# Kernel tuning notes

Measured on AMD Instinct MI355X. Metric: run time of the kernel, lower is better.

## Reference

```python
import jax, jax.numpy as jnp
import numpy as np

GROUPS = 8
EPS = 1e-3  # keras GroupNormalization default epsilon


def group_norm(x, gamma, beta):
    # Keras GroupNormalization(axis=-1): reduce over all non-batch, non-group axes.
    B, L, C = x.shape
    xg = x.reshape(B, L, GROUPS, C // GROUPS)
    mean = jnp.mean(xg, axis=(1, 3), keepdims=True)          # [B,1,G,1]
    var = jnp.var(xg, axis=(1, 3), keepdims=True)
    xn = ((xg - mean) * jax.lax.rsqrt(var + EPS)).reshape(B, L, C)
    return xn * gamma + beta


def setup_inputs() -> dict:
    key = jax.random.key(0)
    ks = jax.random.split(key, 6)
    B, L, C = 8, 2048, 512
    x = jax.random.normal(ks[0], (B, L, C), dtype=jnp.float32)
    s = 0.02
    return {
        "x": x,
        "gamma": jnp.ones((C,), jnp.float32),
        "beta": jnp.zeros((C,), jnp.float32),
        "wq": jax.random.normal(ks[1], (C, C), jnp.float32) * s,
        "bq": jnp.zeros((C,), jnp.float32),
        "wk": jax.random.normal(ks[2], (C, C), jnp.float32) * s,
        "bk": jnp.zeros((C,), jnp.float32),
        "wv": jax.random.normal(ks[3], (C, C), jnp.float32) * s,
        "bv": jnp.zeros((C,), jnp.float32),
        "wp": jax.random.normal(ks[4], (C, C), jnp.float32) * s,
        "bp": jnp.zeros((C,), jnp.float32),
    }


def reference(x, gamma, beta, wq, bq, wk, bk, wv, bv, wp, bp):
    C = x.shape[-1]
    scale = jnp.float32(C) ** -0.5
    h = group_norm(x, gamma, beta)                           # normalized input (also residual!)
    q = h @ wq + bq                                          # [B,L,C]
    k = h @ wk + bk
    v = h @ wv + bv
    attn = jnp.einsum('blc,bLc->blL', q, k) * scale          # [B,L,L]
    attn = jax.nn.softmax(attn, axis=-1)
    o = jnp.einsum('blL,bLc->blc', attn, v)                  # [B,L,C]
    o = o @ wp + bp
    return h + o
```

## Files before the change

### kernel.cpp

```cpp
#include <hip/hip_runtime.h>
#include <hip/hip_bf16.h>
#include <cstdint>

typedef unsigned short ushort_t;
typedef __bf16  bf16x8 __attribute__((ext_vector_type(8)));
typedef float   f32x4  __attribute__((ext_vector_type(4)));

#define L_SEQ 2048
#define C_DIM 512
#define B_SZ  8
#define N_GROUPS 8
#define CG 64

__device__ __forceinline__ float bf2f(ushort_t u) {
    union { uint32_t i; float f; } x; x.i = ((uint32_t)u) << 16; return x.f;
}
__device__ __forceinline__ ushort_t f2bf(float f) {
    union { float f; uint32_t i; } x; x.f = f;
    uint32_t i = x.i;
    uint32_t r = (i + 0x7FFFu + ((i >> 16) & 1u)) >> 16;
    return (ushort_t)r;
}

__device__ __forceinline__ void gl_lds16(const ushort_t* g, ushort_t* l) {
    __builtin_amdgcn_global_load_lds(
        (const __attribute__((address_space(1))) unsigned int*)g,
        (__attribute__((address_space(3))) unsigned int*)l, 16, 0, 0);
}

__global__ __launch_bounds__(256) void conv_stats(const float* __restrict__ wq,
                                                  const float* __restrict__ wk,
                                                  const float* __restrict__ wv,
                                                  const float* __restrict__ wp,
                                                  ushort_t* __restrict__ wqkvT,
                                                  ushort_t* __restrict__ wpT,
                                                  const float* __restrict__ x,
                                                  float* __restrict__ sums) {
    int tid = threadIdx.x;
    if (blockIdx.x < 256) {
        __shared__ ushort_t Ts[64][72];
        int blk = blockIdx.x;
        int mat = blk >> 6, t = blk & 63;
        int k0 = (t >> 3) * 64, n0 = (t & 7) * 64;
        const float* srcs[4] = {wq, wk, wv, wp};
        const float* src = srcs[mat];
        #pragma unroll
        for (int i = 0; i < 2; ++i) {
            int idx = tid * 2 + i;
            int row = idx >> 3, c8 = (idx & 7) * 8;
            const float* p = src + (size_t)(k0 + row) * 512 + n0 + c8;
            float4 a = *(const float4*)p;
            float4 b = *(const float4*)(p + 4);
            Ts[row][c8 + 0] = f2bf(a.x); Ts[row][c8 + 1] = f2bf(a.y);
            Ts[row][c8 + 2] = f2bf(a.z); Ts[row][c8 + 3] = f2bf(a.w);
            Ts[row][c8 + 4] = f2bf(b.x); Ts[row][c8 + 5] = f2bf(b.y);
            Ts[row][c8 + 6] = f2bf(b.z); Ts[row][c8 + 7] = f2bf(b.w);
        }
        __syncthreads();
        int dr = tid >> 2, lc = (tid & 3) * 16;
        union { uint4 v[2]; ushort_t u[16]; } o;
        #pragma unroll
        for (int j = 0; j < 16; ++j) o.u[j] = Ts[lc + j][dr];
        ushort_t* dst = (mat == 3 ? wpT + (size_t)(n0 + dr) * 512
                                  : wqkvT + (size_t)(mat * 512 + n0 + dr) * 512) + k0 + lc;
        *(uint4*)dst = o.v[0];
        *(uint4*)(dst + 8) = o.v[1];
    } else {
        int bid = blockIdx.x - 256;
        int bg = bid >> 3, sp = bid & 7;
        int b = bg >> 3, g = bg & 7;
        const float* base = x + ((size_t)b * L_SEQ + sp * 256) * C_DIM + g * CG;
        float s = 0.f, s2 = 0.f;
        #pragma unroll
        for (int it = 0; it < 8; ++it) {
            int i = it * 2048 + tid * 8;
            int l = i >> 6, c = i & 63;
            const float* p = base + (size_t)l * C_DIM + c;
            float4 a = *(const float4*)p;
            float4 bb = *(const float4*)(p + 4);
            s  += a.x + a.y + a.z + a.w + bb.x + bb.y + bb.z + bb.w;
            s2 += a.x*a.x + a.y*a.y + a.z*a.z + a.w*a.w
                + bb.x*bb.x + bb.y*bb.y + bb.z*bb.z + bb.w*bb.w;
        }
        #pragma unroll
        for (int off = 32; off > 0; off >>= 1) { s += __shfl_down(s, off); s2 += __shfl_down(s2, off); }
        __shared__ float rs[4], rs2[4];
        int wave = tid >> 6;
        if ((tid & 63) == 0) { rs[wave] = s; rs2[wave] = s2; }
        __syncthreads();
        if (tid == 0) {
            sums[bg * 16 + sp * 2 + 0] = rs[0] + rs[1] + rs[2] + rs[3];
            sums[bg * 16 + sp * 2 + 1] = rs2[0] + rs2[1] + rs2[2] + rs2[3];
        }
    }
}

__global__ __launch_bounds__(256) void gn_apply(const float* __restrict__ x,
                                                const float* __restrict__ gamma,
                                                const float* __restrict__ beta,
                                                const float* __restrict__ sums,
                                                ushort_t* __restrict__ h) {
    size_t e = ((size_t)blockIdx.x * 256 + threadIdx.x) * 8;
    int c = (int)(e % C_DIM);
    size_t bl = e / C_DIM;
    int b = (int)(bl / L_SEQ);
    int g = c >> 6;
    int bg = b * 8 + g;
    float s = 0.f, s2 = 0.f;
    #pragma unroll
    for (int sp = 0; sp < 8; ++sp) { s += sums[bg * 16 + sp * 2]; s2 += sums[bg * 16 + sp * 2 + 1]; }
    const float N = (float)(L_SEQ * CG);
    float mean = s / N;
    float var  = s2 / N - mean * mean;
    float rstd = rsqrtf(var + 1e-3f);
    float4 a = *(const float4*)(x + e);
    float4 bb = *(const float4*)(x + e + 4);
    float xf[8] = {a.x, a.y, a.z, a.w, bb.x, bb.y, bb.z, bb.w};
    union { uint4 v; ushort_t u[8]; } o;
    #pragma unroll
    for (int i = 0; i < 8; ++i)
        o.u[i] = f2bf((xf[i] - mean) * rstd * gamma[c + i] + beta[c + i]);
    *(uint4*)(h + e) = o.v;
}

__global__ __launch_bounds__(256) void gemm_qkv(const ushort_t* __restrict__ h,
                                                const ushort_t* __restrict__ wqkvT,
                                                const float* __restrict__ bq,
                                                const float* __restrict__ bk,
                                                const float* __restrict__ bv,
                                                ushort_t* __restrict__ qb,
                                                ushort_t* __restrict__ kb,
                                                ushort_t* __restrict__ vtb) {
    __shared__ ushort_t As[128][64];
    __shared__ ushort_t Bs[128][64];
    int id = blockIdx.x;
    const ushort_t *A, *BT;
    int m0, n0g, vmode;
    if (id < 1024) {
        int swz = (id & 7) * 128 + (id >> 3);
        n0g = (swz & 7) * 128;
        m0  = (swz >> 3) * 128;
        A = h; BT = wqkvT; vmode = 0;
    } else {
        int vid = id - 1024;
        int swz = (vid & 7) * 64 + (vid >> 3);
        n0g = (swz >> 2) * 128;
        m0  = (swz & 3) * 128;
        A = wqkvT + 2 * (size_t)C_DIM * C_DIM; BT = h; vmode = 1;
    }
    int tid = threadIdx.x, lane = tid & 63, w = tid >> 6;
    int l15 = lane & 15, quad = lane >> 4;
    int wm = w >> 1, wn = w & 1;
    int lr8 = lane >> 3;
    int gch = (lane & 7) ^ lr8;
    int h8  = l15 & 7;
    f32x4 acc[4][4] = {};
    for (int k0 = 0; k0 < 512; k0 += 64) {
        #pragma unroll
        for (int j = 0; j < 4; ++j) {
            int rb = w * 32 + j * 8;
            int r  = rb + lr8;
            gl_lds16(A  + (size_t)(m0 + r) * 512 + k0 + gch * 8, &As[rb][0]);
            gl_lds16(BT + (size_t)(n0g + r) * 512 + k0 + gch * 8, &Bs[rb][0]);
        }
        __syncthreads();
        #pragma unroll
        for (int kk = 0; kk < 2; ++kk) {
            int slot = ((quad + 4 * kk) ^ h8) * 8;
            bf16x8 af[4], bf[4];
            #pragma unroll
            for (int t = 0; t < 4; ++t) {
                af[t] = *(const bf16x8*)&As[wm * 64 + t * 16 + l15][slot];
                bf[t] = *(const bf16x8*)&Bs[wn * 64 + t * 16 + l15][slot];
            }
            #pragma unroll
            for (int mt = 0; mt < 4; ++mt)
                #pragma unroll
                for (int nt = 0; nt < 4; ++nt)
                    acc[mt][nt] = __builtin_amdgcn_mfma_f32_16x16x32_bf16(af[mt], bf[nt], acc[mt][nt], 0, 0, 0);
        }
        __syncthreads();
    }
    if (vmode == 0) {
        int seg = n0g >> 9;
        const float* bias = seg ? bk : bq;
        ushort_t* ob = seg ? kb : qb;
        int ns = n0g & 511;
        #pragma unroll
        for (int mt = 0; mt < 4; ++mt)
            #pragma unroll
            for (int nt = 0; nt < 4; ++nt) {
                int n = ns + wn * 64 + nt * 16 + l15;
                float bvn = bias[n];
                #pragma unroll
                for (int r = 0; r < 4; ++r) {
                    int m = m0 + wm * 64 + mt * 16 + quad * 4 + r;
                    ob[(size_t)m * 512 + n] = f2bf(acc[mt][nt][r] + bvn);
                }
            }
    } else {
        #pragma unroll
        for (int mt = 0; mt < 4; ++mt)
            #pragma unroll
            for (int nt = 0; nt < 4; ++nt) {
                int n = n0g + wn * 64 + nt * 16 + l15;
                #pragma unroll
                for (int r = 0; r < 4; ++r) {
                    int m = m0 + wm * 64 + mt * 16 + quad * 4 + r;
                    float v = acc[mt][nt][r] + bv[m];
                    vtb[(size_t)(n >> 11) * 1048576 + (size_t)m * 2048 + (n & 2047)] = f2bf(v);
                }
            }
    }
}

__global__ __launch_bounds__(256) void gemm_proj(const ushort_t* __restrict__ A,
                                                 const ushort_t* __restrict__ BT,
                                                 const float* __restrict__ b0,
                                                 const ushort_t* __restrict__ res,
                                                 float* __restrict__ of) {
    __shared__ ushort_t As[128][64];
    __shared__ ushort_t Bs[128][64];
    int id = blockIdx.x;
    int swz = (id & 7) * 64 + (id >> 3);
    int n0g = (swz & 3) * 128;
    int m0  = (swz >> 2) * 128;
    int tid = threadIdx.x, lane = tid & 63, w = tid >> 6;
    int l15 = lane & 15, quad = lane >> 4;
    int wm = w >> 1, wn = w & 1;
    int lr8 = lane >> 3;
    int gch = (lane & 7) ^ lr8;
    int h8  = l15 & 7;
    f32x4 acc[4][4] = {};
    for (int k0 = 0; k0 < 512; k0 += 64) {
        #pragma unroll
        for (int j = 0; j < 4; ++j) {
            int rb = w * 32 + j * 8;
            int r  = rb + lr8;
            gl_lds16(A  + (size_t)(m0 + r) * 512 + k0 + gch * 8, &As[rb][0]);
            gl_lds16(BT + (size_t)(n0g + r) * 512 + k0 + gch * 8, &Bs[rb][0]);
        }
        __syncthreads();
        #pragma unroll
        for (int kk = 0; kk < 2; ++kk) {
            int slot = ((quad + 4 * kk) ^ h8) * 8;
            bf16x8 af[4], bf[4];
            #pragma unroll
            for (int t = 0; t < 4; ++t) {
                af[t] = *(const bf16x8*)&As[wm * 64 + t * 16 + l15][slot];
                bf[t] = *(const bf16x8*)&Bs[wn * 64 + t * 16 + l15][slot];
            }
            #pragma unroll
            for (int mt = 0; mt < 4; ++mt)
                #pragma unroll
                for (int nt = 0; nt < 4; ++nt)
                    acc[mt][nt] = __builtin_amdgcn_mfma_f32_16x16x32_bf16(af[mt], bf[nt], acc[mt][nt], 0, 0, 0);
        }
        __syncthreads();
    }
    #pragma unroll
    for (int mt = 0; mt < 4; ++mt)
        #pragma unroll
        for (int nt = 0; nt < 4; ++nt) {
            int n = n0g + wn * 64 + nt * 16 + l15;
            float bvn = b0[n];
            #pragma unroll
            for (int r = 0; r < 4; ++r) {
                int m = m0 + wm * 64 + mt * 16 + quad * 4 + r;
                of[(size_t)m * 512 + n] = acc[mt][nt][r] + bvn + bf2f(res[(size_t)m * 512 + n]);
            }
        }
}

__global__ __launch_bounds__(768, 3) void attn11(const ushort_t* __restrict__ Q,
                                                 const ushort_t* __restrict__ K,
                                                 const ushort_t* __restrict__ vT,
                                                 ushort_t* __restrict__ O) {
    __shared__ ushort_t Ks[2][32][520];
    __shared__ ushort_t Vs[2][512][32];
    __shared__ ushort_t Ps[2][64][40];
    __shared__ float    Al[2][64];
    __shared__ float    Lb[64];
    int tid = threadIdx.x;
    int lane = tid & 63, w = tid >> 6;
    int l15 = lane & 15, quad = lane >> 4;
    int b  = blockIdx.x & 7;
    int qt = blockIdx.x >> 3;
    const float scale2 = 0.044194173824159216f * 1.4426950408889634f;
    const ushort_t* Qb = Q + (size_t)b * L_SEQ * C_DIM;
    const ushort_t* Kb = K + (size_t)b * L_SEQ * C_DIM;
    const ushort_t* Vt = vT + (size_t)b * C_DIM * L_SEQ;
    ushort_t* Ob = O + (size_t)b * L_SEQ * C_DIM;

    bool isQK = (w < 4);
    int pw = w - 4;
    int d0 = pw * 64;

    bf16x8 qf[16];
    float m_r = -1e30f, l_r = 0.f;
    f32x4 acc[4][4];

    if (isQK) {
        int qr = qt * 64 + w * 16 + l15;
        #pragma unroll
        for (int ks = 0; ks < 16; ++ks)
            qf[ks] = *(const bf16x8*)(Qb + (size_t)qr * C_DIM + ks * 32 + quad * 8);
    } else {
        #pragma unroll
        for (int qi = 0; qi < 4; ++qi)
            #pragma unroll
            for (int nt = 0; nt < 4; ++nt) acc[qi][nt] = (f32x4){0.f, 0.f, 0.f, 0.f};
        #pragma unroll
        for (int i = 0; i < 4; ++i) {
            int row = pw * 4 + i;
            gl_lds16(Kb + (size_t)row * C_DIM + lane * 8, &Ks[0][row][0]);
        }
    }
    __syncthreads();

    for (int kt = 0; kt <= 64; ++kt) {
        int cur = kt & 1, prv = cur ^ 1;
        if (isQK) {
            if (kt < 64) {
                f32x4 s0a = (f32x4){0.f, 0.f, 0.f, 0.f};
                f32x4 s0b = (f32x4){0.f, 0.f, 0.f, 0.f};
                f32x4 s1a = (f32x4){0.f, 0.f, 0.f, 0.f};
                f32x4 s1b = (f32x4){0.f, 0.f, 0.f, 0.f};
                __builtin_amdgcn_s_setprio(1);
                #pragma unroll
                for (int ks = 0; ks < 16; ks += 2) {
                    bf16x8 kf0 = *(const bf16x8*)&Ks[cur][l15][ks * 32 + quad * 8];
                    bf16x8 kf1 = *(const bf16x8*)&Ks[cur][16 + l15][ks * 32 + quad * 8];
                    bf16x8 kf2 = *(const bf16x8*)&Ks[cur][l15][(ks + 1) * 32 + quad * 8];
                    bf16x8 kf3 = *(const bf16x8*)&Ks[cur][16 + l15][(ks + 1) * 32 + quad * 8];
                    s0a = __builtin_amdgcn_mfma_f32_16x16x32_bf16(kf0, qf[ks], s0a, 0, 0, 0);
                    s1a = __builtin_amdgcn_mfma_f32_16x16x32_bf16(kf1, qf[ks], s1a, 0, 0, 0);
                    s0b = __builtin_amdgcn_mfma_f32_16x16x32_bf16(kf2, qf[ks + 1], s0b, 0, 0, 0);
                    s1b = __builtin_amdgcn_mfma_f32_16x16x32_bf16(kf3, qf[ks + 1], s1b, 0, 0, 0);
                }
                __builtin_amdgcn_s_setprio(0);
                f32x4 s0 = s0a + s0b;
                f32x4 s1 = s1a + s1b;
                float mx = fmaxf(fmaxf(fmaxf(s0[0], s0[1]), fmaxf(s0[2], s0[3])),
                                 fmaxf(fmaxf(s1[0], s1[1]), fmaxf(s1[2], s1[3])));
                mx = fmaxf(mx, __shfl_xor(mx, 16, 64));
                mx = fmaxf(mx, __shfl_xor(mx, 32, 64));
                mx *= scale2;
                float mn = fmaxf(m_r, mx);
                float alpha = exp2f(m_r - mn);
                m_r = mn;
                ushort_t pb[8];
                float rs = 0.f;
                #pragma unroll
                for (int r = 0; r < 4; ++r) {
                    pb[r]     = f2bf(exp2f(s0[r] * scale2 - mn));
                    pb[4 + r] = f2bf(exp2f(s1[r] * scale2 - mn));
                    rs += bf2f(pb[r]) + bf2f(pb[4 + r]);
                }
                rs += __shfl_xor(rs, 16, 64);
                rs += __shfl_xor(rs, 32, 64);
                l_r = l_r * alpha + rs;
                int row = w * 16 + l15;
                uint2 w0, w1;
                w0.x = (uint32_t)pb[0] | ((uint32_t)pb[1] << 16);
                w0.y = (uint32_t)pb[2] | ((uint32_t)pb[3] << 16);
                w1.x = (uint32_t)pb[4] | ((uint32_t)pb[5] << 16);
                w1.y = (uint32_t)pb[6] | ((uint32_t)pb[7] << 16);
                *(uint2*)&Ps[cur][row][quad * 4] = w0;
                *(uint2*)&Ps[cur][row][16 + quad * 4] = w1;
                if (lane < 16) Al[cur][w * 16 + lane] = alpha;
            } else {
                if (lane < 16) Lb[w * 16 + lane] = l_r;
            }
        } else {
            if (kt < 63) {
                #pragma unroll
                for (int i = 0; i < 4; ++i) {
                    int row = pw * 4 + i;
                    gl_lds16(Kb + (size_t)((kt + 1) * 32 + row) * C_DIM + lane * 8, &Ks[prv][row][0]);
                }
            }
            if (kt < 64) {
                int k0 = kt * 32;
                #pragma unroll
                for (int i = 0; i < 4; ++i) {
                    int r0 = (pw * 4 + i) * 16;
                    gl_lds16(Vt + (size_t)(r0 + (lane >> 2)) * L_SEQ + k0 + (lane & 3) * 8,
                             &Vs[cur][r0][0]);
                }
            }
            if (kt > 0) {
                bf16x8 pf[4];
                #pragma unroll
                for (int qi = 0; qi < 4; ++qi)
                    pf[qi] = *(const bf16x8*)&Ps[prv][qi * 16 + l15][quad * 8];
                #pragma unroll
                for (int qi = 0; qi < 4; ++qi) {
                    float4 av = *(const float4*)&Al[prv][qi * 16 + quad * 4];
                    #pragma unroll
                    for (int nt = 0; nt < 4; ++nt) {
                        acc[qi][nt][0] *= av.x; acc[qi][nt][1] *= av.y;
                        acc[qi][nt][2] *= av.z; acc[qi][nt][3] *= av.w;
                    }
                }
                bf16x8 vf[4];
                #pragma unroll
                for (int nt = 0; nt < 4; ++nt)
                    vf[nt] = *(const bf16x8*)&Vs[prv][d0 + nt * 16 + l15][quad * 8];
                __builtin_amdgcn_s_setprio(1);
                #pragma unroll
                for (int nt = 0; nt < 4; ++nt)
                    #pragma unroll
                    for (int qi = 0; qi < 4; ++qi)
                        acc[qi][nt] = __builtin_amdgcn_mfma_f32_16x16x32_bf16(pf[qi], vf[nt], acc[qi][nt], 0, 0, 0);
                __builtin_amdgcn_s_setprio(0);
            }
        }
        __syncthreads();
    }
    if (!isQK) {
        #pragma unroll
        for (int qi = 0; qi < 4; ++qi) {
            float4 lv = *(const float4*)&Lb[qi * 16 + quad * 4];
            float inv[4] = {1.f / lv.x, 1.f / lv.y, 1.f / lv.z, 1.f / lv.w};
            #pragma unroll
            for (int r = 0; r < 4; ++r) {
                int m = qt * 64 + qi * 16 + quad * 4 + r;
                #pragma unroll
                for (int nt = 0; nt < 4; ++nt)
                    Ob[(size_t)m * 512 + d0 + nt * 16 + l15] = f2bf(acc[qi][nt][r] * inv[r]);
            }
        }
    }
}

extern "C" void kernel_launch(void* const* d_in, const int* in_sizes, int n_in,
                              void* d_out, int out_size, void* d_ws, size_t ws_size,
                              hipStream_t stream) {
    const float* x     = (const float*)d_in[0];
    const float* gamma = (const float*)d_in[1];
    const float* beta  = (const float*)d_in[2];
    const float* wq    = (const float*)d_in[3];
    const float* bq    = (const float*)d_in[4];
    const float* wk    = (const float*)d_in[5];
    const float* bk    = (const float*)d_in[6];
    const float* wv    = (const float*)d_in[7];
    const float* bv    = (const float*)d_in[8];
    const float* wp    = (const float*)d_in[9];
    const float* bp    = (const float*)d_in[10];
    float* out = (float*)d_out;

    const size_t MC = (size_t)B_SZ * L_SEQ * C_DIM;
    const size_t WC = (size_t)C_DIM * C_DIM;
    ushort_t* h     = (ushort_t*)d_ws;
    ushort_t* qb    = h     + MC;
    ushort_t* kb    = qb    + MC;
    ushort_t* vbuf  = kb    + MC;
    ushort_t* vtb   = vbuf  + MC;
    ushort_t* wqkvT = vtb   + MC;
    ushort_t* wpT   = wqkvT + 3 * WC;
    float* sums     = (float*)(wpT + WC);

    conv_stats<<<dim3(768), dim3(256), 0, stream>>>(wq, wk, wv, wp, wqkvT, wpT, x, sums);
    gn_apply<<<dim3(4096), dim3(256), 0, stream>>>(x, gamma, beta, sums, h);

    gemm_qkv<<<dim3(1536), dim3(256), 0, stream>>>(h, wqkvT, bq, bk, bv, qb, kb, vtb);

    attn11<<<dim3(256), dim3(768), 0, stream>>>(qb, kb, vtb, vbuf);

    gemm_proj<<<dim3(512), dim3(256), 0, stream>>>(vbuf, wpT, bp, h, out);
}
```

Baseline: 307.7 us.

## Double-buffer LDS tiles in QKV and projection GEMMs with K-step of 32

Result: slower. 324.1 us (+5.3%).

```diff
diff --git a/kernel.cpp b/kernel.cpp
--- a/kernel.cpp
+++ b/kernel.cpp
@@ -131,8 +131,8 @@
                                                 ushort_t* __restrict__ qb,
                                                 ushort_t* __restrict__ kb,
                                                 ushort_t* __restrict__ vtb) {
-    __shared__ ushort_t As[128][64];
-    __shared__ ushort_t Bs[128][64];
+    __shared__ ushort_t As[2][128][32];
+    __shared__ ushort_t Bs[2][128][32];
     int id = blockIdx.x;
     const ushort_t *A, *BT;
     int m0, n0g, vmode;
@@ -151,34 +151,38 @@
     int tid = threadIdx.x, lane = tid & 63, w = tid >> 6;
     int l15 = lane & 15, quad = lane >> 4;
     int wm = w >> 1, wn = w & 1;
-    int lr8 = lane >> 3;
-    int gch = (lane & 7) ^ lr8;
-    int h8  = l15 & 7;
+    int sr = lane >> 2;
+    int sc = (lane & 3) * 8;
     f32x4 acc[4][4] = {};
-    for (int k0 = 0; k0 < 512; k0 += 64) {
-        #pragma unroll
-        for (int j = 0; j < 4; ++j) {
-            int rb = w * 32 + j * 8;
-            int r  = rb + lr8;
-            gl_lds16(A  + (size_t)(m0 + r) * 512 + k0 + gch * 8, &As[rb][0]);
-            gl_lds16(BT + (size_t)(n0g + r) * 512 + k0 + gch * 8, &Bs[rb][0]);
-        }
-        __syncthreads();
-        #pragma unroll
-        for (int kk = 0; kk < 2; ++kk) {
-            int slot = ((quad + 4 * kk) ^ h8) * 8;
-            bf16x8 af[4], bf[4];
-            #pragma unroll
-            for (int t = 0; t < 4; ++t) {
-                af[t] = *(const bf16x8*)&As[wm * 64 + t * 16 + l15][slot];
-                bf[t] = *(const bf16x8*)&Bs[wn * 64 + t * 16 + l15][slot];
-            }
-            #pragma unroll
-            for (int mt = 0; mt < 4; ++mt)
-                #pragma unroll
-                for (int nt = 0; nt < 4; ++nt)
-                    acc[mt][nt] = __builtin_amdgcn_mfma_f32_16x16x32_bf16(af[mt], bf[nt], acc[mt][nt], 0, 0, 0);
-        }
+    #pragma unroll
+    for (int j = 0; j < 2; ++j) {
+        int rb = j * 64 + w * 16;
+        gl_lds16(A  + (size_t)(m0  + rb + sr) * 512 + sc, &As[0][rb][0]);
+        gl_lds16(BT + (size_t)(n0g + rb + sr) * 512 + sc, &Bs[0][rb][0]);
+    }
+    __syncthreads();
+    for (int kt = 0; kt < 16; ++kt) {
+        int cur = kt & 1;
+        if (kt < 15) {
+            int k0 = (kt + 1) * 32;
+            #pragma unroll
+            for (int j = 0; j < 2; ++j) {
+                int rb = j * 64 + w * 16;
+                gl_lds16(A  + (size_t)(m0  + rb + sr) * 512 + k0 + sc, &As[cur ^ 1][rb][0]);
+                gl_lds16(BT + (size_t)(n0g + rb + sr) * 512 + k0 + sc, &Bs[cur ^ 1][rb][0]);
+            }
+        }
+        bf16x8 af[4], bf[4];
+        #pragma unroll
+        for (int t = 0; t < 4; ++t) {
+            af[t] = *(const bf16x8*)&As[cur][wm * 64 + t * 16 + l15][quad * 8];
+            bf[t] = *(const bf16x8*)&Bs[cur][wn * 64 + t * 16 + l15][quad * 8];
+        }
+        #pragma unroll
+        for (int mt = 0; mt < 4; ++mt)
+            #pragma unroll
+            for (int nt = 0; nt < 4; ++nt)
+                acc[mt][nt] = __builtin_amdgcn_mfma_f32_16x16x32_bf16(af[mt], bf[nt], acc[mt][nt], 0, 0, 0);
         __syncthreads();
     }
     if (vmode == 0) {
@@ -219,8 +223,8 @@
                                                  const float* __restrict__ b0,
                                                  const ushort_t* __restrict__ res,
                                                  float* __restrict__ of) {
-    __shared__ ushort_t As[128][64];
-    __shared__ ushort_t Bs[128][64];
+    __shared__ ushort_t As[2][128][32];
+    __shared__ ushort_t Bs[2][128][32];
     int id = blockIdx.x;
     int swz = (id & 7) * 64 + (id >> 3);
     int n0g = (swz & 3) * 128;
@@ -228,34 +232,38 @@
     int tid = threadIdx.x, lane = tid & 63, w = tid >> 6;
     int l15 = lane & 15, quad = lane >> 4;
     int wm = w >> 1, wn = w & 1;
-    int lr8 = lane >> 3;
-    int gch = (lane & 7) ^ lr8;
-    int h8  = l15 & 7;
+    int sr = lane >> 2;
+    int sc = (lane & 3) * 8;
     f32x4 acc[4][4] = {};
-    for (int k0 = 0; k0 < 512; k0 += 64) {
-        #pragma unroll
-        for (int j = 0; j < 4; ++j) {
-            int rb = w * 32 + j * 8;
-            int r  = rb + lr8;
-            gl_lds16(A  + (size_t)(m0 + r) * 512 + k0 + gch * 8, &As[rb][0]);
-            gl_lds16(BT + (size_t)(n0g + r) * 512 + k0 + gch * 8, &Bs[rb][0]);
-        }
-        __syncthreads();
-        #pragma unroll
-        for (int kk = 0; kk < 2; ++kk) {
-            int slot = ((quad + 4 * kk) ^ h8) * 8;
-            bf16x8 af[4], bf[4];
-            #pragma unroll
-            for (int t = 0; t < 4; ++t) {
-                af[t] = *(const bf16x8*)&As[wm * 64 + t * 16 + l15][slot];
-                bf[t] = *(const bf16x8*)&Bs[wn * 64 + t * 16 + l15][slot];
-            }
-            #pragma unroll
-            for (int mt = 0; mt < 4; ++mt)
-                #pragma unroll
-                for (int nt = 0; nt < 4; ++nt)
-                    acc[mt][nt] = __builtin_amdgcn_mfma_f32_16x16x32_bf16(af[mt], bf[nt], acc[mt][nt], 0, 0, 0);
-        }
+    #pragma unroll
+    for (int j = 0; j < 2; ++j) {
+        int rb = j * 64 + w * 16;
+        gl_lds16(A  + (size_t)(m0  + rb + sr) * 512 + sc, &As[0][rb][0]);
+        gl_lds16(BT + (size_t)(n0g + rb + sr) * 512 + sc, &Bs[0][rb][0]);
+    }
+    __syncthreads();
+    for (int kt = 0; kt < 16; ++kt) {
+        int cur = kt & 1;
+        if (kt < 15) {
+            int k0 = (kt + 1) * 32;
+            #pragma unroll
+            for (int j = 0; j < 2; ++j) {
+                int rb = j * 64 + w * 16;
+                gl_lds16(A  + (size_t)(m0  + rb + sr) * 512 + k0 + sc, &As[cur ^ 1][rb][0]);
+                gl_lds16(BT + (size_t)(n0g + rb + sr) * 512 + k0 + sc, &Bs[cur ^ 1][rb][0]);
+            }
+        }
+        bf16x8 af[4], bf[4];
+        #pragma unroll
+        for (int t = 0; t < 4; ++t) {
+            af[t] = *(const bf16x8*)&As[cur][wm * 64 + t * 16 + l15][quad * 8];
+            bf[t] = *(const bf16x8*)&Bs[cur][wn * 64 + t * 16 + l15][quad * 8];
+        }
+        #pragma unroll
+        for (int mt = 0; mt < 4; ++mt)
+            #pragma unroll
+            for (int nt = 0; nt < 4; ++nt)
+                acc[mt][nt] = __builtin_amdgcn_mfma_f32_16x16x32_bf16(af[mt], bf[nt], acc[mt][nt], 0, 0, 0);
         __syncthreads();
     }
     #pragma unroll
```
